# Optimization experiments

Measured on AMD Instinct MI355X. Metric: run time of the kernel, lower is better.

The kernel has to match this reference:

```python
import jax, jax.numpy as jnp
import numpy as np

B, L, D = 4, 4096, 1024
H, M = 16, 256
DH = D // H  # 64


def setup_inputs() -> dict:
    key = jax.random.key(0)
    ks = jax.random.split(key, 7)
    s = 1.0 / np.sqrt(D).astype(np.float32)  # keep activations O(1) so exp() stays sane
    x = jax.random.normal(ks[0], (B, L, D), dtype=jnp.float32)
    Wq = jax.random.normal(ks[1], (D, D), dtype=jnp.float32) * s
    Wk = jax.random.normal(ks[2], (D, D), dtype=jnp.float32) * s
    Wv = jax.random.normal(ks[3], (D, D), dtype=jnp.float32) * s
    Wo = jax.random.normal(ks[4], (D, D), dtype=jnp.float32) * s
    bo = jnp.zeros((D,), dtype=jnp.float32)
    omega = jax.random.normal(ks[5], (DH, M), dtype=jnp.float32)
    return {"x": x, "Wq": Wq, "Wk": Wk, "Wv": Wv, "Wo": Wo, "bo": bo, "omega": omega}


def _phi(x, omega):
    # x: (B,H,L,dh) -> positive random features (B,H,L,m)
    scale = DH ** 0.25
    x_s = x / scale
    proj = jnp.einsum('bhld,dm->bhlm', x_s, omega)
    norm_sq = jnp.sum(x_s * x_s, axis=-1, keepdims=True) * 0.5
    return jnp.exp(proj - norm_sq) / (M ** 0.5)


def reference(x, Wq, Wk, Wv, Wo, bo, omega):
    # nn.Linear: y = x @ W.T
    def heads(W):
        return (x @ W.T).reshape(B, L, H, DH).transpose(0, 2, 1, 3)
    Q, K, V = heads(Wq), heads(Wk), heads(Wv)
    Q_feat = _phi(Q, omega)   # (B,H,L,m)
    K_feat = _phi(K, omega)   # (B,H,L,m)
    KV = jnp.einsum('bhlm,bhld->bhmd', K_feat, V)      # (B,H,m,dh)
    out = jnp.einsum('bhlm,bhmd->bhld', Q_feat, KV)    # (B,H,L,dh)
    K_sum = K_feat.sum(axis=2)                          # (B,H,m)
    norm = jnp.einsum('bhlm,bhm->bhl', Q_feat, K_sum)
    norm = jnp.clip(norm, 1e-6, None)[..., None]
    out = out / norm
    out = out.transpose(0, 2, 1, 3).reshape(B, L, D)
    return out @ Wo.T + bo
```

## Files before the change

kernel.cpp:

```cpp
#include <hip/hip_runtime.h>

typedef unsigned short u16;
typedef __attribute__((ext_vector_type(4))) float f32x4;
typedef _Float16 f16x8 __attribute__((ext_vector_type(8)));
typedef __attribute__((ext_vector_type(4))) u16   u16x4;
typedef __attribute__((ext_vector_type(8))) u16   u16x8;

#define DEV static __device__ __forceinline__

constexpr int Ll = 4096;

DEV float h2f(u16 v) { _Float16 h; __builtin_memcpy(&h, &v, 2); return (float)h; }
DEV u16 f2h(float f) { _Float16 h = (_Float16)f; u16 u; __builtin_memcpy(&u, &h, 2); return u; }

DEV f32x4 mfma16h(f16x8 a, f16x8 b, f32x4 c) {
    return __builtin_amdgcn_mfma_f32_16x16x32_f16(a, b, c, 0, 0, 0);
}

#if defined(__has_builtin)
#if __has_builtin(__builtin_amdgcn_global_load_lds)
#define HAS_GLLDS 1
#endif
#endif
#ifndef HAS_GLLDS
#define HAS_GLLDS 0
#endif

#define SBAR()  __builtin_amdgcn_s_barrier()
#define SCHED() __builtin_amdgcn_sched_barrier(0)
#define LGKM0() asm volatile("s_waitcnt lgkmcnt(0)" ::: "memory")

#if HAS_GLLDS
#define STG2(BUF, REG, SRC, ROWBASE, TK, KS)                                         \
  { _Pragma("unroll") for (int u_ = 0; u_ < 2; u_++) {                               \
      int row_ = u_ * 128 + wave * 16 + (lane >> 2);                                 \
      int c_ = lane & 3;                                                             \
      const u16* gp_ = (SRC) + (size_t)((ROWBASE) + row_) * 1024 + (TK) * 64         \
                        + (KS) * 32 + ((c_ ^ ((row_ >> 1) & 3)) * 8);                \
      __builtin_amdgcn_global_load_lds(                                              \
        (const __attribute__((address_space(1))) unsigned int*)gp_,                  \
        (__attribute__((address_space(3))) unsigned int*)(sm + (BUF) * 32768 +       \
          (REG) * 8192 + (u_ * 512 + wave * 64) * 8), 16, 0, 0); } }
#else
#define STG2(BUF, REG, SRC, ROWBASE, TK, KS)                                         \
  { _Pragma("unroll") for (int u_ = 0; u_ < 2; u_++) {                               \
      int row_ = u_ * 128 + wave * 16 + (lane >> 2);                                 \
      int c_ = lane & 3;                                                             \
      const u16* gp_ = (SRC) + (size_t)((ROWBASE) + row_) * 1024 + (TK) * 64         \
                        + (KS) * 32 + ((c_ ^ ((row_ >> 1) & 3)) * 8);                \
      *(u16x8*)(sm + (BUF) * 32768 + (REG) * 8192 + (u_ * 512 + wave * 64 + lane) * 8) \
          = *(const u16x8*)gp_; } }
#endif

#if HAS_GLLDS
#define STG(BUF, U, SRC, ROWBASE, KK)                                                \
  { int rl_ = wave * 16 + (lane >> 2);                                               \
    int c_ = lane & 3;                                                               \
    int grow_ = (((U) & 1) * 128) + rl_;                                             \
    const u16* gp_ = (SRC) + (size_t)((ROWBASE) + grow_) * 1024 + (KK)               \
                     + ((c_ ^ ((rl_ >> 1) & 3)) * 8);                                \
    __builtin_amdgcn_global_load_lds(                                                \
        (const __attribute__((address_space(1))) unsigned int*)gp_,                  \
        (__attribute__((address_space(3))) unsigned int*)(sm + (BUF) * 16384 +       \
            (U) * 4096 + wave * 512), 16, 0, 0); }
#else
#define STG(BUF, U, SRC, ROWBASE, KK)                                                \
  { int rl_ = wave * 16 + (lane >> 2);                                               \
    int c_ = lane & 3;                                                               \
    int grow_ = (((U) & 1) * 128) + rl_;                                             \
    const u16* gp_ = (SRC) + (size_t)((ROWBASE) + grow_) * 1024 + (KK)               \
                     + ((c_ ^ ((rl_ >> 1) & 3)) * 8);                                \
    *(u16x8*)(sm + (BUF) * 16384 + (U) * 4096 + wave * 512 + lane * 8)               \
        = *(const u16x8*)gp_; }
#endif

__global__ __launch_bounds__(256) void k_prep(
    const float* __restrict__ x, const float* __restrict__ Wq, const float* __restrict__ Wk,
    const float* __restrict__ Wv, const float* __restrict__ Wo, const float* __restrict__ om,
    u16* __restrict__ xh, u16* __restrict__ Wc, u16* __restrict__ wtp) {
    int bx = blockIdx.x, tid = threadIdx.x;
    if (bx < 16384) {
        size_t i = ((size_t)bx * 256 + tid) * 4;
        f32x4 v = *(const f32x4*)(x + i);
        u16x4 h;
#pragma unroll
        for (int j = 0; j < 4; j++) h[j] = f2h(v[j]);
        *(u16x4*)(xh + i) = h;
    } else if (bx < 20480) {
        int wsel = (bx - 16384) >> 10;
        const float* src = (wsel == 0) ? Wq : (wsel == 1) ? Wk : (wsel == 2) ? Wv : Wo;
        size_t i = ((size_t)((bx - 16384) & 1023) * 256 + tid) * 4;
        f32x4 v = *(const f32x4*)(src + i);
        u16x4 h;
#pragma unroll
        for (int j = 0; j < 4; j++) h[j] = f2h(v[j]);
        *(u16x4*)(Wc + (size_t)wsel * 1048576 + i) = h;
    } else {
        int i = (bx - 20480) * 256 + tid;
        int m = i >> 6, d = i & 63;
        wtp[i] = f2h(om[d * 256 + m] * 0.35355339059327373f);
    }
}

__global__ __launch_bounds__(512, 1) void k_gemm_qkv(
    const u16* __restrict__ Ax, const u16* __restrict__ Bw,
    u16* __restrict__ QK, u16* __restrict__ Vb) {
    __shared__ __align__(16) u16 sm[65536];
    const int tid = threadIdx.x, wave = tid >> 6, lane = tid & 63;
    const int lr = lane & 15, lkq = lane >> 4;
    const int wr = wave >> 2, wc = wave & 3;
    const int m0 = blockIdx.y * 256, n0 = blockIdx.x * 256;
    const int sec = n0 >> 10;

    const int arow = wr * 128 + lr;
    const int aBase = arow * 32 + ((lkq ^ ((arow >> 1) & 3)) * 8);
    const int brow = wc * 64 + lr;
    const int bBase = 16384 + brow * 32 + ((lkq ^ ((brow >> 1) & 3)) * 8);

    f32x4 acc[8][4];
#pragma unroll
    for (int i = 0; i < 8; i++)
#pragma unroll
        for (int j = 0; j < 4; j++)
#pragma unroll
            for (int r = 0; r < 4; r++) acc[i][j][r] = 0.f;

    STG2(0, 0, Ax, m0, 0, 0)
    STG2(0, 2, Bw, n0, 0, 0)
    STG2(0, 1, Ax, m0, 0, 1)
    STG2(0, 3, Bw, n0, 0, 1)
    asm volatile("s_waitcnt vmcnt(4)" ::: "memory");
    SCHED(); SBAR(); SCHED();

    f16x8 bfr[2][4], afr[4];
    for (int t = 0; t < 16; ++t) {
        const u16* bp = sm + (t & 1) * 32768;
        const int nb = (t + 1) & 1;
        const bool st = t < 15;
#pragma unroll
        for (int f = 0; f < 4; f++) afr[f] = *(const f16x8*)&bp[aBase + f * 512];
#pragma unroll
        for (int j = 0; j < 4; j++) bfr[0][j] = *(const f16x8*)&bp[bBase + j * 512];
        if (st) STG2(nb, 0, Ax, m0, t + 1, 0)
        SBAR(); LGKM0(); SCHED();
        __builtin_amdgcn_s_setprio(1);
#pragma unroll
        for (int i = 0; i < 4; i++)
#pragma unroll
            for (int j = 0; j < 4; j++)
                acc[i][j] = mfma16h(afr[i], bfr[0][j], acc[i][j]);
        __builtin_amdgcn_s_setprio(0);
        SCHED();
        if (st) { asm volatile("s_waitcnt vmcnt(2)" ::: "memory"); }
        else    { asm volatile("s_waitcnt vmcnt(0)" ::: "memory"); }
        SCHED(); SBAR(); SCHED();
#pragma unroll
        for (int f = 0; f < 4; f++) afr[f] = *(const f16x8*)&bp[aBase + 8192 + f * 512];
#pragma unroll
        for (int j = 0; j < 4; j++) bfr[1][j] = *(const f16x8*)&bp[bBase + 8192 + j * 512];
        if (st) STG2(nb, 2, Bw, n0, t + 1, 0)
        SBAR(); LGKM0(); SCHED();
        __builtin_amdgcn_s_setprio(1);
#pragma unroll
        for (int i = 0; i < 4; i++)
#pragma unroll
            for (int j = 0; j < 4; j++)
                acc[i][j] = mfma16h(afr[i], bfr[1][j], acc[i][j]);
        __builtin_amdgcn_s_setprio(0);
        SCHED(); SBAR(); SCHED();
#pragma unroll
        for (int f = 0; f < 4; f++) afr[f] = *(const f16x8*)&bp[aBase + 2048 + f * 512];
        if (st) STG2(nb, 1, Ax, m0, t + 1, 1)
        SBAR(); LGKM0(); SCHED();
        __builtin_amdgcn_s_setprio(1);
#pragma unroll
        for (int i = 0; i < 4; i++)
#pragma unroll
            for (int j = 0; j < 4; j++)
                acc[4 + i][j] = mfma16h(afr[i], bfr[0][j], acc[4 + i][j]);
        __builtin_amdgcn_s_setprio(0);
        SCHED(); SBAR(); SCHED();
#pragma unroll
        for (int f = 0; f < 4; f++) afr[f] = *(const f16x8*)&bp[aBase + 8192 + 2048 + f * 512];
        if (st) STG2(nb, 3, Bw, n0, t + 1, 1)
        SBAR(); LGKM0(); SCHED();
        __builtin_amdgcn_s_setprio(1);
#pragma unroll
        for (int i = 0; i < 4; i++)
#pragma unroll
            for (int j = 0; j < 4; j++)
                acc[4 + i][j] = mfma16h(afr[i], bfr[1][j], acc[4 + i][j]);
        __builtin_amdgcn_s_setprio(0);
        SCHED();
        if (st) { asm volatile("s_waitcnt vmcnt(4)" ::: "memory"); }
        SCHED(); SBAR(); SCHED();
    }

    float* ep = (float*)sm;
    for (int g = 0; g < 8; g++) {
        __syncthreads();
        if (wr == (g >> 2)) {
#pragma unroll
            for (int fi = 0; fi < 2; fi++) {
                int fm = (g & 3) * 2 + fi;
#pragma unroll
                for (int fn = 0; fn < 4; fn++)
#pragma unroll
                    for (int r = 0; r < 4; r++)
                        ep[(fi * 16 + (lane >> 4) * 4 + r) * 264 + wc * 64 + fn * 16 + lr] = acc[fm][fn][r];
            }
        }
        __syncthreads();
        int row = tid >> 4, c0 = (tid & 15) * 16;
        int grow = m0 + g * 32 + row;
        u16x8 h0, h1;
#pragma unroll
        for (int j = 0; j < 8; j++) {
            h0[j] = f2h(ep[row * 264 + c0 + j]);
            h1[j] = f2h(ep[row * 264 + c0 + 8 + j]);
        }
        if (sec < 2) {
            size_t o = (size_t)grow * 2048 + (n0 + c0);
            *(u16x8*)(QK + o) = h0; *(u16x8*)(QK + o + 8) = h1;
        } else {
            size_t o = (size_t)grow * 1024 + (n0 - 2048 + c0);
            *(u16x8*)(Vb + o) = h0; *(u16x8*)(Vb + o + 8) = h1;
        }
    }
}

__global__ __launch_bounds__(512, 2) void k_gemm_out(
    const u16* __restrict__ Ab, const u16* __restrict__ Bw,
    const float* __restrict__ bias, float* __restrict__ outp) {
    __shared__ __align__(16) u16 sm[32768];
    const int tid = threadIdx.x, wave = tid >> 6, lane = tid & 63;
    const int lr = lane & 15, lkq = lane >> 4;
    const int wr = wave >> 2, wc = wave & 3;
    const int m0 = blockIdx.y * 256, n0 = blockIdx.x * 256;

    int aoff[8], boff[4];
#pragma unroll
    for (int f = 0; f < 8; f++) {
        int row = wr * 128 + f * 16 + lr;
        aoff[f] = row * 32 + ((lkq ^ ((row >> 1) & 3)) * 8);
    }
#pragma unroll
    for (int f = 0; f < 4; f++) {
        int row = wc * 64 + f * 16 + lr;
        boff[f] = row * 32 + ((lkq ^ ((row >> 1) & 3)) * 8);
    }

    f32x4 acc[8][4];
#pragma unroll
    for (int i = 0; i < 8; i++)
#pragma unroll
        for (int j = 0; j < 4; j++)
#pragma unroll
            for (int r = 0; r < 4; r++) acc[i][j][r] = 0.f;

    STG(0, 0, Ab, m0, 0) STG(0, 1, Ab, m0, 0)
    STG(0, 2, Bw, n0, 0) STG(0, 3, Bw, n0, 0)
    asm volatile("s_waitcnt vmcnt(0)" ::: "memory");
    SCHED(); SBAR(); SCHED();

    int cb = 0;
    for (int t = 0; t < 32; ++t) {
        const u16* Abase = sm + cb * 16384;
        const u16* Bbase = Abase + 8192;
        f16x8 afr[4], bfr[4];
#pragma unroll
        for (int f = 0; f < 4; f++) bfr[f] = *(const f16x8*)&Bbase[boff[f]];
#pragma unroll
        for (int f = 0; f < 4; f++) afr[f] = *(const f16x8*)&Abase[aoff[f]];
        if (t < 31) {
            int kk = (t + 1) * 32;
            STG(cb ^ 1, 0, Ab, m0, kk) STG(cb ^ 1, 1, Ab, m0, kk)
            STG(cb ^ 1, 2, Bw, n0, kk) STG(cb ^ 1, 3, Bw, n0, kk)
        }
        SCHED(); SBAR(); LGKM0(); SCHED();
        __builtin_amdgcn_s_setprio(1);
#pragma unroll
        for (int i = 0; i < 4; i++)
#pragma unroll
            for (int j = 0; j < 4; j++)
                acc[i][j] = mfma16h(afr[i], bfr[j], acc[i][j]);
        __builtin_amdgcn_s_setprio(0);
        SCHED(); SBAR(); SCHED();
#pragma unroll
        for (int f = 0; f < 4; f++) afr[f] = *(const f16x8*)&Abase[aoff[4 + f]];
        SCHED(); SBAR(); LGKM0(); SCHED();
        __builtin_amdgcn_s_setprio(1);
#pragma unroll
        for (int i = 0; i < 4; i++)
#pragma unroll
            for (int j = 0; j < 4; j++)
                acc[4 + i][j] = mfma16h(afr[i], bfr[j], acc[4 + i][j]);
        __builtin_amdgcn_s_setprio(0);
        asm volatile("s_waitcnt vmcnt(0)" ::: "memory");
        SCHED(); SBAR(); SCHED();
        cb ^= 1;
    }

    float* ep = (float*)sm;
    for (int g = 0; g < 8; g++) {
        __syncthreads();
        if (wr == (g >> 2)) {
#pragma unroll
            for (int fi = 0; fi < 2; fi++) {
                int fm = (g & 3) * 2 + fi;
#pragma unroll
                for (int fn = 0; fn < 4; fn++)
#pragma unroll
                    for (int r = 0; r < 4; r++)
                        ep[(fi * 16 + (lane >> 4) * 4 + r) * 264 + wc * 64 + fn * 16 + lr] = acc[fm][fn][r];
            }
        }
        __syncthreads();
        int row = tid >> 4, c0 = (tid & 15) * 16;
        int grow = m0 + g * 32 + row;
        float vv[16];
#pragma unroll
        for (int j = 0; j < 16; j++) vv[j] = ep[row * 264 + c0 + j] + bias[n0 + c0 + j];
#pragma unroll
        for (int p = 0; p < 4; p++) {
            f32x4 tv;
#pragma unroll
            for (int q = 0; q < 4; q++) tv[q] = vv[p * 4 + q];
            *(f32x4*)(outp + (size_t)grow * 1024 + n0 + c0 + p * 4) = tv;
        }
    }
}

__global__ __launch_bounds__(256) void k_phik_kv(
    const u16* __restrict__ QK, const u16* __restrict__ wt,
    const u16* __restrict__ Vb, float* __restrict__ KVacc, float* __restrict__ Ksum) {
    __shared__ __align__(16) u16 sKh[64 * 72];
    __shared__ __align__(16) u16 sVt[64 * 72];
    __shared__ __align__(16) u16 sKfT[256 * 72];
    __shared__ float snsq[64];
    const int tid = threadIdx.x, wave = tid >> 6, lane = tid & 63;
    const int lr = lane & 15, lk = (lane >> 4) * 8;
    const int kc = blockIdx.x, bh = blockIdx.y;
    const int b = bh >> 4, h = bh & 15;

    f16x8 wb[4][2];
#pragma unroll
    for (int fn = 0; fn < 4; fn++)
#pragma unroll
        for (int ks = 0; ks < 2; ks++)
            wb[fn][ks] = *(const f16x8*)(wt + (size_t)(wave * 64 + fn * 16 + lr) * 64 + ks * 32 + lk);

    f32x4 akv[4][4];
#pragma unroll
    for (int i = 0; i < 4; i++)
#pragma unroll
        for (int j = 0; j < 4; j++)
#pragma unroll
            for (int r = 0; r < 4; r++) akv[i][j][r] = 0.f;
    float ksm[4] = {0.f, 0.f, 0.f, 0.f};

    const int rowS = tid >> 2, cS = (tid & 3) * 16;
    size_t gK = ((size_t)(b * Ll + kc * 512 + rowS)) * 2048 + 1024 + h * 64 + cS;
    size_t gV = ((size_t)(b * Ll + kc * 512 + rowS)) * 1024 + h * 64 + cS;
    u16x8 kh0 = *(const u16x8*)(QK + gK);
    u16x8 kh1 = *(const u16x8*)(QK + gK + 8);
    u16x8 vv0 = *(const u16x8*)(Vb + gV);
    u16x8 vv1 = *(const u16x8*)(Vb + gV + 8);

    for (int it = 0; it < 8; it++) {
        __syncthreads();
        {
            *(u16x8*)&sKh[rowS * 72 + cS]     = kh0;
            *(u16x8*)&sKh[rowS * 72 + cS + 8] = kh1;
            float s = 0.f;
#pragma unroll
            for (int j = 0; j < 8; j++) {
                float a = h2f(kh0[j]); s += a * a;
                float c = h2f(kh1[j]); s += c * c;
            }
            s += __shfl_xor(s, 1); s += __shfl_xor(s, 2);
            if ((tid & 3) == 0) snsq[rowS] = s * 0.0625f;
        }
        {
#pragma unroll
            for (int j = 0; j < 8; j++) {
                sVt[(cS + j) * 72 + rowS]     = vv0[j];
                sVt[(cS + 8 + j) * 72 + rowS] = vv1[j];
            }
        }
        __syncthreads();
        if (it < 7) {
            gK += 131072; gV += 65536;
            kh0 = *(const u16x8*)(QK + gK);
            kh1 = *(const u16x8*)(QK + gK + 8);
            vv0 = *(const u16x8*)(Vb + gV);
            vv1 = *(const u16x8*)(Vb + gV + 8);
        }
#pragma unroll
        for (int fm = 0; fm < 4; fm++) {
            f32x4 ap[4];
#pragma unroll
            for (int fn = 0; fn < 4; fn++)
#pragma unroll
                for (int r = 0; r < 4; r++) ap[fn][r] = 0.f;
#pragma unroll
            for (int ks = 0; ks < 2; ks++) {
                f16x8 aH = *(const f16x8*)&sKh[(fm * 16 + lr) * 72 + ks * 32 + lk];
#pragma unroll
                for (int fn = 0; fn < 4; fn++)
                    ap[fn] = mfma16h(aH, wb[fn][ks], ap[fn]);
            }
#pragma unroll
            for (int fn = 0; fn < 4; fn++) {
                u16x4 pk;
#pragma unroll
                for (int r = 0; r < 4; r++) {
                    float ns = snsq[fm * 16 + (lane >> 4) * 4 + r];
                    float val = __expf(ap[fn][r] - ns) * 0.00390625f;
                    ksm[fn] += val;
                    pk[r] = f2h(val);
                }
                *(u16x4*)&sKfT[(wave * 64 + fn * 16 + lr) * 72 + fm * 16 + (lane >> 4) * 4] = pk;
            }
        }
#pragma unroll
        for (int ks = 0; ks < 2; ks++) {
            f16x8 a4[4], b4[4];
#pragma unroll
            for (int f = 0; f < 4; f++) {
                a4[f] = *(const f16x8*)&sKfT[(wave * 64 + f * 16 + lr) * 72 + ks * 32 + lk];
                b4[f] = *(const f16x8*)&sVt[(f * 16 + lr) * 72 + ks * 32 + lk];
            }
#pragma unroll
            for (int fm = 0; fm < 4; fm++)
#pragma unroll
                for (int fn = 0; fn < 4; fn++)
                    akv[fm][fn] = mfma16h(a4[fm], b4[fn], akv[fm][fn]);
        }
    }
    const size_t base = ((size_t)(kc * 64 + bh)) << 14;
#pragma unroll
    for (int fm = 0; fm < 4; fm++)
#pragma unroll
        for (int fn = 0; fn < 4; fn++)
#pragma unroll
            for (int r = 0; r < 4; r++) {
                int m = wave * 64 + fm * 16 + (lane >> 4) * 4 + r;
                int d = fn * 16 + lr;
                KVacc[base + m * 64 + d] = akv[fm][fn][r];
            }
#pragma unroll
    for (int fn = 0; fn < 4; fn++) {
        ksm[fn] += __shfl_xor(ksm[fn], 16);
        ksm[fn] += __shfl_xor(ksm[fn], 32);
    }
    if (lane < 16) {
#pragma unroll
        for (int fn = 0; fn < 4; fn++)
            Ksum[(kc * 64 + bh) * 256 + wave * 64 + fn * 16 + lane] = ksm[fn];
    }
}

__global__ __launch_bounds__(256) void k_kvt(const float* __restrict__ KVacc,
                                             const float* __restrict__ Ksum,
                                             u16* __restrict__ KVt, float* __restrict__ KsumR) {
    int i = blockIdx.x * 256 + threadIdx.x;
    if (blockIdx.x < 16384) {
        int bh = i >> 14, m = (i >> 6) & 255, d = i & 63;
        float s = 0.f;
#pragma unroll
        for (int kc = 0; kc < 8; kc++)
            s += KVacc[(((size_t)(kc * 64 + bh)) << 14) + m * 64 + d];
        KVt[((size_t)bh << 14) + d * 256 + m] = f2h(s);
    } else {
        int j = i - 4194304;
        int bh = j >> 8, m = j & 255;
        float s = 0.f;
#pragma unroll
        for (int kc = 0; kc < 8; kc++)
            s += Ksum[(kc * 64 + bh) * 256 + m];
        KsumR[j] = s;
    }
}

__global__ __launch_bounds__(512) void k_phiq_attn(
    const u16* __restrict__ QK, const u16* __restrict__ wt,
    const u16* __restrict__ KVt, const float* __restrict__ Ksum,
    u16* __restrict__ attn) {
    __shared__ __align__(16) u16 sQh[64 * 72];
    __shared__ __align__(16) u16 sQf[64 * 264];
    __shared__ float sKs[256];
    __shared__ float snsq[64];
    __shared__ float snorm[64];
    const int tid = threadIdx.x, wave = tid >> 6, lane = tid & 63;
    const int lr = lane & 15, lk = (lane >> 4) * 8;
    const int bh = blockIdx.y, b = bh >> 4, h = bh & 15;
    const int mq = wave & 3;
    const int lh = wave >> 2;
    const int af = wave & 3;
    const int ad = wave >> 2;

    f16x8 wb[4][2];
#pragma unroll
    for (int fn = 0; fn < 4; fn++)
#pragma unroll
        for (int ks = 0; ks < 2; ks++)
            wb[fn][ks] = *(const f16x8*)(wt + (size_t)(mq * 64 + fn * 16 + lr) * 64 + ks * 32 + lk);
    f16x8 kvb[2][8];
#pragma unroll
    for (int fn = 0; fn < 2; fn++)
#pragma unroll
        for (int ks = 0; ks < 8; ks++)
            kvb[fn][ks] = *(const f16x8*)(KVt + ((size_t)bh << 14) +
                                          (size_t)(ad * 32 + fn * 16 + lr) * 256 + ks * 32 + lk);
    if (tid < 256) sKs[tid] = Ksum[bh * 256 + tid];

    const int rowQ = tid >> 3, cQ = (tid & 7) * 8;
    size_t gQ = ((size_t)(b * Ll + blockIdx.x * 256 + rowQ)) * 2048 + h * 64 + cQ;
    u16x8 vh = *(const u16x8*)(QK + gQ);

    for (int st = 0; st < 4; st++) {
        const int l0 = blockIdx.x * 256 + st * 64;
        __syncthreads();
        {
            *(u16x8*)&sQh[rowQ * 72 + cQ] = vh;
            float s = 0.f;
#pragma unroll
            for (int j = 0; j < 8; j++) { float a = h2f(vh[j]); s += a * a; }
            s += __shfl_xor(s, 1); s += __shfl_xor(s, 2); s += __shfl_xor(s, 4);
            if ((tid & 7) == 0) snsq[rowQ] = s * 0.0625f;
        }
        __syncthreads();
#pragma unroll
        for (int fm = 0; fm < 2; fm++) {
            f32x4 ap[4];
#pragma unroll
            for (int fn = 0; fn < 4; fn++)
#pragma unroll
                for (int r = 0; r < 4; r++) ap[fn][r] = 0.f;
#pragma unroll
            for (int ks = 0; ks < 2; ks++) {
                f16x8 aH = *(const f16x8*)&sQh[(lh * 32 + fm * 16 + lr) * 72 + ks * 32 + lk];
#pragma unroll
                for (int fn = 0; fn < 4; fn++)
                    ap[fn] = mfma16h(aH, wb[fn][ks], ap[fn]);
            }
#pragma unroll
            for (int fn = 0; fn < 4; fn++)
#pragma unroll
                for (int r = 0; r < 4; r++) {
                    int l = lh * 32 + fm * 16 + (lane >> 4) * 4 + r;
                    int m = mq * 64 + fn * 16 + lr;
                    sQf[l * 264 + m] = f2h(__expf(ap[fn][r] - snsq[l]) * 0.0625f);
                }
        }
        if (st < 3) {
            gQ += 131072;
            vh = *(const u16x8*)(QK + gQ);
        }
        __syncthreads();
        {
            int l = tid >> 3, m0 = (tid & 7) * 32;
            float s = 0.f;
#pragma unroll
            for (int j4 = 0; j4 < 4; j4++) {
                u16x8 qv = *(const u16x8*)&sQf[l * 264 + m0 + j4 * 8];
#pragma unroll
                for (int j = 0; j < 8; j++) s += h2f(qv[j]) * sKs[m0 + j4 * 8 + j];
            }
            s += __shfl_xor(s, 1); s += __shfl_xor(s, 2); s += __shfl_xor(s, 4);
            if ((tid & 7) == 0) snorm[l] = s;
        }
        f32x4 aa[2];
#pragma unroll
        for (int fn = 0; fn < 2; fn++)
#pragma unroll
            for (int r = 0; r < 4; r++) aa[fn][r] = 0.f;
#pragma unroll
        for (int ks = 0; ks < 8; ks++) {
            f16x8 a = *(const f16x8*)&sQf[(af * 16 + lr) * 264 + ks * 32 + lk];
            aa[0] = mfma16h(a, kvb[0][ks], aa[0]);
            aa[1] = mfma16h(a, kvb[1][ks], aa[1]);
        }
        __syncthreads();
        float* ep = (float*)sQf;
#pragma unroll
        for (int fn = 0; fn < 2; fn++)
#pragma unroll
            for (int r = 0; r < 4; r++) {
                int l = af * 16 + (lane >> 4) * 4 + r;
                int d = ad * 32 + fn * 16 + lr;
                ep[l * 68 + d] = aa[fn][r];
            }
        __syncthreads();
        {
            int l = tid >> 3, d0 = (tid & 7) * 8;
            float inv = 1.0f / fmaxf(snorm[l], 6.25e-8f);
            u16x8 o;
#pragma unroll
            for (int j = 0; j < 8; j++) o[j] = f2h(ep[l * 68 + d0 + j] * inv);
            *(u16x8*)(attn + ((size_t)(b * Ll + l0 + l)) * 1024 + h * 64 + d0) = o;
        }
    }
}

extern "C" void kernel_launch(void* const* d_in, const int* in_sizes, int n_in,
                              void* d_out, int out_size, void* d_ws, size_t ws_size,
                              hipStream_t stream) {
    (void)in_sizes; (void)n_in; (void)out_size; (void)ws_size;
    const float* x  = (const float*)d_in[0];
    const float* Wq = (const float*)d_in[1];
    const float* Wk = (const float*)d_in[2];
    const float* Wv = (const float*)d_in[3];
    const float* Wo = (const float*)d_in[4];
    const float* bo = (const float*)d_in[5];
    const float* om = (const float*)d_in[6];

    char* w = (char*)d_ws;
    size_t o = 0;
    auto take = [&](size_t n) { char* p = w + o; o += n; return p; };
    u16* QK  = (u16*)take(67108864);
    u16* Vb  = (u16*)take(33554432);
    u16* xh  = (u16*)take(33554432);
    u16* Wc  = (u16*)take(8388608);
    u16* wt  = (u16*)take(32768);
    float* KVacc = (float*)take(33554432);
    float* Ksum  = (float*)take(524288);
    float* KsumR = (float*)take(65536);
    u16* KVt = (u16*)take(2097152);
    u16* Wof  = Wc + 3145728;
    u16* attn = Vb;

    k_prep<<<20544, 256, 0, stream>>>(x, Wq, Wk, Wv, Wo, om, xh, Wc, wt);
    k_gemm_qkv<<<dim3(12, 64), 512, 0, stream>>>(xh, Wc, QK, Vb);
    k_phik_kv<<<dim3(8, 64), 256, 0, stream>>>(QK, wt, Vb, KVacc, Ksum);
    k_kvt<<<16448, 256, 0, stream>>>(KVacc, Ksum, KVt, KsumR);
    k_phiq_attn<<<dim3(16, 64), 512, 0, stream>>>(QK, wt, KVt, KsumR, attn);
    k_gemm_out<<<dim3(4, 64), 512, 0, stream>>>(attn, Wof, bo, (float*)d_out);
}
```

Before: 369.6 us.

## Restructure output GEMM pipeline and double K-split in phi-K/KV kernel

The output projection GEMM moves to K=64 tiles in a 128KB LDS double buffer using the STG2 staging macro, with loads issued in quarter-steps between MFMA phases and partial vmcnt waits. Occupancy drops to one block per CU in exchange for fewer barriers per K step. The phi-K/KV kernel now splits L into 16 chunks instead of 8 and processes the feature transpose in half-size tiles to cut LDS use. This doubles the KV partial-sum workspace and the reduction work in k_kvt.

```diff
diff --git a/kernel.cpp b/kernel.cpp
--- a/kernel.cpp
+++ b/kernel.cpp
@@ -52,28 +52,6 @@
           = *(const u16x8*)gp_; } }
 #endif
 
-#if HAS_GLLDS
-#define STG(BUF, U, SRC, ROWBASE, KK)                                                \
-  { int rl_ = wave * 16 + (lane >> 2);                                               \
-    int c_ = lane & 3;                                                               \
-    int grow_ = (((U) & 1) * 128) + rl_;                                             \
-    const u16* gp_ = (SRC) + (size_t)((ROWBASE) + grow_) * 1024 + (KK)               \
-                     + ((c_ ^ ((rl_ >> 1) & 3)) * 8);                                \
-    __builtin_amdgcn_global_load_lds(                                                \
-        (const __attribute__((address_space(1))) unsigned int*)gp_,                  \
-        (__attribute__((address_space(3))) unsigned int*)(sm + (BUF) * 16384 +       \
-            (U) * 4096 + wave * 512), 16, 0, 0); }
-#else
-#define STG(BUF, U, SRC, ROWBASE, KK)                                                \
-  { int rl_ = wave * 16 + (lane >> 2);                                               \
-    int c_ = lane & 3;                                                               \
-    int grow_ = (((U) & 1) * 128) + rl_;                                             \
-    const u16* gp_ = (SRC) + (size_t)((ROWBASE) + grow_) * 1024 + (KK)               \
-                     + ((c_ ^ ((rl_ >> 1) & 3)) * 8);                                \
-    *(u16x8*)(sm + (BUF) * 16384 + (U) * 4096 + wave * 512 + lane * 8)               \
-        = *(const u16x8*)gp_; }
-#endif
-
 __global__ __launch_bounds__(256) void k_prep(
     const float* __restrict__ x, const float* __restrict__ Wq, const float* __restrict__ Wk,
     const float* __restrict__ Wv, const float* __restrict__ Wo, const float* __restrict__ om,
@@ -229,26 +207,19 @@
     }
 }
 
-__global__ __launch_bounds__(512, 2) void k_gemm_out(
+__global__ __launch_bounds__(512, 1) void k_gemm_out(
     const u16* __restrict__ Ab, const u16* __restrict__ Bw,
     const float* __restrict__ bias, float* __restrict__ outp) {
-    __shared__ __align__(16) u16 sm[32768];
+    __shared__ __align__(16) u16 sm[65536];
     const int tid = threadIdx.x, wave = tid >> 6, lane = tid & 63;
     const int lr = lane & 15, lkq = lane >> 4;
     const int wr = wave >> 2, wc = wave & 3;
     const int m0 = blockIdx.y * 256, n0 = blockIdx.x * 256;
 
-    int aoff[8], boff[4];
-#pragma unroll
-    for (int f = 0; f < 8; f++) {
-        int row = wr * 128 + f * 16 + lr;
-        aoff[f] = row * 32 + ((lkq ^ ((row >> 1) & 3)) * 8);
-    }
-#pragma unroll
-    for (int f = 0; f < 4; f++) {
-        int row = wc * 64 + f * 16 + lr;
-        boff[f] = row * 32 + ((lkq ^ ((row >> 1) & 3)) * 8);
-    }
+    const int arow = wr * 128 + lr;
+    const int aBase = arow * 32 + ((lkq ^ ((arow >> 1) & 3)) * 8);
+    const int brow = wc * 64 + lr;
+    const int bBase = 16384 + brow * 32 + ((lkq ^ ((brow >> 1) & 3)) * 8);
 
     f32x4 acc[8][4];
 #pragma unroll
@@ -258,47 +229,75 @@
 #pragma unroll
             for (int r = 0; r < 4; r++) acc[i][j][r] = 0.f;
 
-    STG(0, 0, Ab, m0, 0) STG(0, 1, Ab, m0, 0)
-    STG(0, 2, Bw, n0, 0) STG(0, 3, Bw, n0, 0)
-    asm volatile("s_waitcnt vmcnt(0)" ::: "memory");
+    STG2(0, 0, Ab, m0, 0, 0)
+    STG2(0, 2, Bw, n0, 0, 0)
+    STG2(0, 1, Ab, m0, 0, 1)
+    STG2(0, 3, Bw, n0, 0, 1)
+    asm volatile("s_waitcnt vmcnt(4)" ::: "memory");
     SCHED(); SBAR(); SCHED();
 
-    int cb = 0;
-    for (int t = 0; t < 32; ++t) {
-        const u16* Abase = sm + cb * 16384;
-        const u16* Bbase = Abase + 8192;
-        f16x8 afr[4], bfr[4];
-#pragma unroll
-        for (int f = 0; f < 4; f++) bfr[f] = *(const f16x8*)&Bbase[boff[f]];
-#pragma unroll
-        for (int f = 0; f < 4; f++) afr[f] = *(const f16x8*)&Abase[aoff[f]];
-        if (t < 31) {
-            int kk = (t + 1) * 32;
-            STG(cb ^ 1, 0, Ab, m0, kk) STG(cb ^ 1, 1, Ab, m0, kk)
-            STG(cb ^ 1, 2, Bw, n0, kk) STG(cb ^ 1, 3, Bw, n0, kk)
-        }
-        SCHED(); SBAR(); LGKM0(); SCHED();
-        __builtin_amdgcn_s_setprio(1);
-#pragma unroll
-        for (int i = 0; i < 4; i++)
-#pragma unroll
-            for (int j = 0; j < 4; j++)
-                acc[i][j] = mfma16h(afr[i], bfr[j], acc[i][j]);
-        __builtin_amdgcn_s_setprio(0);
-        SCHED(); SBAR(); SCHED();
-#pragma unroll
-        for (int f = 0; f < 4; f++) afr[f] = *(const f16x8*)&Abase[aoff[4 + f]];
-        SCHED(); SBAR(); LGKM0(); SCHED();
-        __builtin_amdgcn_s_setprio(1);
-#pragma unroll
-        for (int i = 0; i < 4; i++)
-#pragma unroll
-            for (int j = 0; j < 4; j++)
-                acc[4 + i][j] = mfma16h(afr[i], bfr[j], acc[4 + i][j]);
-        __builtin_amdgcn_s_setprio(0);
-        asm volatile("s_waitcnt vmcnt(0)" ::: "memory");
-        SCHED(); SBAR(); SCHED();
-        cb ^= 1;
+    f16x8 bfr[2][4], afr[4];
+    for (int t = 0; t < 16; ++t) {
+        const u16* bp = sm + (t & 1) * 32768;
+        const int nb = (t + 1) & 1;
+        const bool st = t < 15;
+#pragma unroll
+        for (int f = 0; f < 4; f++) afr[f] = *(const f16x8*)&bp[aBase + f * 512];
+#pragma unroll
+        for (int j = 0; j < 4; j++) bfr[0][j] = *(const f16x8*)&bp[bBase + j * 512];
+        if (st) STG2(nb, 0, Ab, m0, t + 1, 0)
+        SBAR(); LGKM0(); SCHED();
+        __builtin_amdgcn_s_setprio(1);
+#pragma unroll
+        for (int i = 0; i < 4; i++)
+#pragma unroll
+            for (int j = 0; j < 4; j++)
+                acc[i][j] = mfma16h(afr[i], bfr[0][j], acc[i][j]);
+        __builtin_amdgcn_s_setprio(0);
+        SCHED();
+        if (st) { asm volatile("s_waitcnt vmcnt(2)" ::: "memory"); }
+        else    { asm volatile("s_waitcnt vmcnt(0)" ::: "memory"); }
+        SCHED(); SBAR(); SCHED();
+#pragma unroll
+        for (int f = 0; f < 4; f++) afr[f] = *(const f16x8*)&bp[aBase + 8192 + f * 512];
+#pragma unroll
+        for (int j = 0; j < 4; j++) bfr[1][j] = *(const f16x8*)&bp[bBase + 8192 + j * 512];
+        if (st) STG2(nb, 2, Bw, n0, t + 1, 0)
+        SBAR(); LGKM0(); SCHED();
+        __builtin_amdgcn_s_setprio(1);
+#pragma unroll
+        for (int i = 0; i < 4; i++)
+#pragma unroll
+            for (int j = 0; j < 4; j++)
+                acc[i][j] = mfma16h(afr[i], bfr[1][j], acc[i][j]);
+        __builtin_amdgcn_s_setprio(0);
+        SCHED(); SBAR(); SCHED();
+#pragma unroll
+        for (int f = 0; f < 4; f++) afr[f] = *(const f16x8*)&bp[aBase + 2048 + f * 512];
+        if (st) STG2(nb, 1, Ab, m0, t + 1, 1)
+        SBAR(); LGKM0(); SCHED();
+        __builtin_amdgcn_s_setprio(1);
+#pragma unroll
+        for (int i = 0; i < 4; i++)
+#pragma unroll
+            for (int j = 0; j < 4; j++)
+                acc[4 + i][j] = mfma16h(afr[i], bfr[0][j], acc[4 + i][j]);
+        __builtin_amdgcn_s_setprio(0);
+        SCHED(); SBAR(); SCHED();
+#pragma unroll
+        for (int f = 0; f < 4; f++) afr[f] = *(const f16x8*)&bp[aBase + 8192 + 2048 + f * 512];
+        if (st) STG2(nb, 3, Bw, n0, t + 1, 1)
+        SBAR(); LGKM0(); SCHED();
+        __builtin_amdgcn_s_setprio(1);
+#pragma unroll
+        for (int i = 0; i < 4; i++)
+#pragma unroll
+            for (int j = 0; j < 4; j++)
+                acc[4 + i][j] = mfma16h(afr[i], bfr[1][j], acc[4 + i][j]);
+        __builtin_amdgcn_s_setprio(0);
+        SCHED();
+        if (st) { asm volatile("s_waitcnt vmcnt(4)" ::: "memory"); }
+        SCHED(); SBAR(); SCHED();
     }
 
     float* ep = (float*)sm;
@@ -336,7 +335,7 @@
     const u16* __restrict__ Vb, float* __restrict__ KVacc, float* __restrict__ Ksum) {
     __shared__ __align__(16) u16 sKh[64 * 72];
     __shared__ __align__(16) u16 sVt[64 * 72];
-    __shared__ __align__(16) u16 sKfT[256 * 72];
+    __shared__ __align__(16) u16 sKfT[256 * 36];
     __shared__ float snsq[64];
     const int tid = threadIdx.x, wave = tid >> 6, lane = tid & 63;
     const int lr = lane & 15, lk = (lane >> 4) * 8;
@@ -360,14 +359,14 @@
     float ksm[4] = {0.f, 0.f, 0.f, 0.f};
 
     const int rowS = tid >> 2, cS = (tid & 3) * 16;
-    size_t gK = ((size_t)(b * Ll + kc * 512 + rowS)) * 2048 + 1024 + h * 64 + cS;
-    size_t gV = ((size_t)(b * Ll + kc * 512 + rowS)) * 1024 + h * 64 + cS;
+    size_t gK = ((size_t)(b * Ll + kc * 256 + rowS)) * 2048 + 1024 + h * 64 + cS;
+    size_t gV = ((size_t)(b * Ll + kc * 256 + rowS)) * 1024 + h * 64 + cS;
     u16x8 kh0 = *(const u16x8*)(QK + gK);
     u16x8 kh1 = *(const u16x8*)(QK + gK + 8);
     u16x8 vv0 = *(const u16x8*)(Vb + gV);
     u16x8 vv1 = *(const u16x8*)(Vb + gV + 8);
 
-    for (int it = 0; it < 8; it++) {
+    for (int it = 0; it < 4; it++) {
         __syncthreads();
         {
             *(u16x8*)&sKh[rowS * 72 + cS]     = kh0;
@@ -389,7 +388,7 @@
             }
         }
         __syncthreads();
-        if (it < 7) {
+        if (it < 3) {
             gK += 131072; gV += 65536;
             kh0 = *(const u16x8*)(QK + gK);
             kh1 = *(const u16x8*)(QK + gK + 8);
@@ -397,39 +396,40 @@
             vv1 = *(const u16x8*)(Vb + gV + 8);
         }
 #pragma unroll
-        for (int fm = 0; fm < 4; fm++) {
-            f32x4 ap[4];
-#pragma unroll
-            for (int fn = 0; fn < 4; fn++)
-#pragma unroll
-                for (int r = 0; r < 4; r++) ap[fn][r] = 0.f;
-#pragma unroll
-            for (int ks = 0; ks < 2; ks++) {
-                f16x8 aH = *(const f16x8*)&sKh[(fm * 16 + lr) * 72 + ks * 32 + lk];
+        for (int p = 0; p < 2; p++) {
+#pragma unroll
+            for (int fm2 = 0; fm2 < 2; fm2++) {
+                int fm = p * 2 + fm2;
+                f32x4 ap[4];
 #pragma unroll
                 for (int fn = 0; fn < 4; fn++)
-                    ap[fn] = mfma16h(aH, wb[fn][ks], ap[fn]);
-            }
-#pragma unroll
-            for (int fn = 0; fn < 4; fn++) {
-                u16x4 pk;
-#pragma unroll
-                for (int r = 0; r < 4; r++) {
-                    float ns = snsq[fm * 16 + (lane >> 4) * 4 + r];
-                    float val = __expf(ap[fn][r] - ns) * 0.00390625f;
-                    ksm[fn] += val;
-                    pk[r] = f2h(val);
+#pragma unroll
+                    for (int r = 0; r < 4; r++) ap[fn][r] = 0.f;
+#pragma unroll
+                for (int ks = 0; ks < 2; ks++) {
+                    f16x8 aH = *(const f16x8*)&sKh[(fm * 16 + lr) * 72 + ks * 32 + lk];
+#pragma unroll
+                    for (int fn = 0; fn < 4; fn++)
+                        ap[fn] = mfma16h(aH, wb[fn][ks], ap[fn]);
                 }
-                *(u16x4*)&sKfT[(wave * 64 + fn * 16 + lr) * 72 + fm * 16 + (lane >> 4) * 4] = pk;
-            }
-        }
-#pragma unroll
-        for (int ks = 0; ks < 2; ks++) {
+#pragma unroll
+                for (int fn = 0; fn < 4; fn++) {
+                    u16x4 pk;
+#pragma unroll
+                    for (int r = 0; r < 4; r++) {
+                        float ns = snsq[fm * 16 + (lane >> 4) * 4 + r];
+                        float val = __expf(ap[fn][r] - ns) * 0.00390625f;
+                        ksm[fn] += val;
+                        pk[r] = f2h(val);
+                    }
+                    *(u16x4*)&sKfT[(wave * 64 + fn * 16 + lr) * 36 + fm2 * 16 + (lane >> 4) * 4] = pk;
+                }
+            }
             f16x8 a4[4], b4[4];
 #pragma unroll
             for (int f = 0; f < 4; f++) {
-                a4[f] = *(const f16x8*)&sKfT[(wave * 64 + f * 16 + lr) * 72 + ks * 32 + lk];
-                b4[f] = *(const f16x8*)&sVt[(f * 16 + lr) * 72 + ks * 32 + lk];
+                a4[f] = *(const f16x8*)&sKfT[(wave * 64 + f * 16 + lr) * 36 + lk];
+                b4[f] = *(const f16x8*)&sVt[(f * 16 + lr) * 72 + p * 32 + lk];
             }
 #pragma unroll
             for (int fm = 0; fm < 4; fm++)
@@ -469,7 +469,7 @@
         int bh = i >> 14, m = (i >> 6) & 255, d = i & 63;
         float s = 0.f;
 #pragma unroll
-        for (int kc = 0; kc < 8; kc++)
+        for (int kc = 0; kc < 16; kc++)
             s += KVacc[(((size_t)(kc * 64 + bh)) << 14) + m * 64 + d];
         KVt[((size_t)bh << 14) + d * 256 + m] = f2h(s);
     } else {
@@ -477,7 +477,7 @@
         int bh = j >> 8, m = j & 255;
         float s = 0.f;
 #pragma unroll
-        for (int kc = 0; kc < 8; kc++)
+        for (int kc = 0; kc < 16; kc++)
             s += Ksum[(kc * 64 + bh) * 256 + m];
         KsumR[j] = s;
     }
@@ -624,8 +624,8 @@
     u16* xh  = (u16*)take(33554432);
     u16* Wc  = (u16*)take(8388608);
     u16* wt  = (u16*)take(32768);
-    float* KVacc = (float*)take(33554432);
-    float* Ksum  = (float*)take(524288);
+    float* KVacc = (float*)take(67108864);
+    float* Ksum  = (float*)take(1048576);
     float* KsumR = (float*)take(65536);
     u16* KVt = (u16*)take(2097152);
     u16* Wof  = Wc + 3145728;
@@ -633,7 +633,7 @@
 
     k_prep<<<20544, 256, 0, stream>>>(x, Wq, Wk, Wv, Wo, om, xh, Wc, wt);
     k_gemm_qkv<<<dim3(12, 64), 512, 0, stream>>>(xh, Wc, QK, Vb);
-    k_phik_kv<<<dim3(8, 64), 256, 0, stream>>>(QK, wt, Vb, KVacc, Ksum);
+    k_phik_kv<<<dim3(16, 64), 256, 0, stream>>>(QK, wt, Vb, KVacc, Ksum);
     k_kvt<<<16448, 256, 0, stream>>>(KVacc, Ksum, KVt, KsumR);
     k_phiq_attn<<<dim3(16, 64), 512, 0, stream>>>(QK, wt, KVt, KsumR, attn);
     k_gemm_out<<<dim3(4, 64), 512, 0, stream>>>(attn, Wof, bo, (float*)d_out);
```

After: 377.3 us. 1.02x slower.
